# Performance work log

Hardware: AMD Instinct MI355X
Metric: run time of the kernel (lower is better)

## Reference

```python
import jax, jax.numpy as jnp
import numpy as np

N_NODES = 100000
N_EDGES = 1600000
C = 64


def _spline_conv(x, src, dst, u, w, root, bias, n_nodes):
    """SplineConv, dim=1, kernel_size=2, degree=1, open spline, aggr='mean'.

    For K=2, degree=1, pseudo u in [0,1]: basis = (1-u) on knot 0, u on knot 1.
    message_e = (1-u_e) * x[src_e] @ w[0] + u_e * x[src_e] @ w[1]
    Compute the two GEMMs at node level (N < E) then gather, which is
    mathematically identical and cheaper.
    """
    h0 = x @ w[0]  # [N, C]
    h1 = x @ w[1]  # [N, C]
    uc = u[:, None]  # [E, 1]
    msg = (1.0 - uc) * h0[src] + uc * h1[src]  # [E, C]
    agg = jax.ops.segment_sum(msg, dst, num_segments=n_nodes)  # [N, C]
    deg = jax.ops.segment_sum(jnp.ones_like(u), dst, num_segments=n_nodes)
    agg = agg / jnp.maximum(deg, 1.0)[:, None]  # mean aggregation
    return agg + x @ root + bias


def setup_inputs() -> dict:
    key = jax.random.key(0)
    ks = jax.random.split(key, 10)
    x = jax.random.normal(ks[0], (N_NODES, C), dtype=jnp.float32)
    edge_index = jax.random.randint(ks[1], (2, N_EDGES), 0, N_NODES, dtype=jnp.int64)
    edge_attr = jax.random.uniform(ks[2], (N_EDGES, 1), dtype=jnp.float32)
    s = 1.0 / np.sqrt(C)
    w1 = jax.random.uniform(ks[3], (2, C, C), jnp.float32, -s, s)
    root1 = jax.random.uniform(ks[4], (C, C), jnp.float32, -s, s)
    b1 = jnp.zeros((C,), jnp.float32)
    w2 = jax.random.uniform(ks[5], (2, C, C), jnp.float32, -s, s)
    root2 = jax.random.uniform(ks[6], (C, C), jnp.float32, -s, s)
    b2 = jnp.zeros((C,), jnp.float32)
    return {"x": x, "edge_index": edge_index, "edge_attr": edge_attr,
            "w1": w1, "root1": root1, "b1": b1,
            "w2": w2, "root2": root2, "b2": b2}


def reference(x, edge_index, edge_attr, w1, root1, b1, w2, root2, b2):
    src, dst = edge_index[0], edge_index[1]
    u = edge_attr[:, 0]
    n = x.shape[0]
    h = _spline_conv(x, src, dst, u, w1, root1, b1, n)
    h = _spline_conv(h, src, dst, u, w2, root2, b2, n)
    return h
```

## Files before the change

### kernel.cpp

```cpp
#include <hip/hip_runtime.h>

#define CDIM 64

typedef __attribute__((ext_vector_type(8))) short bf16x8;
typedef __attribute__((ext_vector_type(4))) float f32x4;

__device__ __forceinline__ short bf16r(float f) {
    unsigned a = __float_as_uint(f);
    a = (a + 0x7fffu + ((a >> 16) & 1u)) >> 16;
    return (short)a;
}
__device__ __forceinline__ unsigned bfpack(float lo, float hi) {
    unsigned a = __float_as_uint(lo);
    a = (a + 0x7fffu + ((a >> 16) & 1u)) >> 16;
    unsigned b = __float_as_uint(hi);
    b = (b + 0x7fffu + ((b >> 16) & 1u)) & 0xffff0000u;
    return a | b;
}

__global__ __launch_bounds__(256) void k_pack(const float* __restrict__ x,
                                              unsigned* __restrict__ xb32, size_t n2) {
    size_t t = (size_t)blockIdx.x * 256 + threadIdx.x;
    size_t stride = (size_t)gridDim.x * 256;
    for (size_t i = t; i < n2; i += stride) {
        float2 v = ((const float2*)x)[i];
        xb32[i] = bfpack(v.x, v.y);
    }
}

#define NPB_SHIFT 9
#define BKN (1 << NPB_SHIFT)
#define BPAD 10240
#define PART_CH 2048
#define RCAP 1536

__global__ __launch_bounds__(256) void k_prep(int* __restrict__ bkt_cursor, int n_buckets,
                                              const float* __restrict__ w1,
                                              const float* __restrict__ root1,
                                              const float* __restrict__ w2,
                                              const float* __restrict__ root2,
                                              short* __restrict__ wtg) {
    int tid = threadIdx.x;
    if (blockIdx.x == 0) {
        if (tid < n_buckets) bkt_cursor[tid] = tid * BPAD;
        return;
    }
    int l = blockIdx.x - 1;
    const float* s0 = l ? w2 : w1;
    const float* srcs[3] = {s0, s0 + 4096, l ? root2 : root1};
    short* o = wtg + (size_t)l * 3 * 4096;
    for (int i = tid; i < 12288; i += 256) {
        int m = i >> 12, r = i & 4095, k = r >> 6, n = r & 63;
        o[(m << 12) + (n << 6) + k] = bf16r(srcs[m][r]);
    }
}

__global__ __launch_bounds__(256) void k_part(const int* __restrict__ src,
                                              const int* __restrict__ dst,
                                              const float* __restrict__ u,
                                              int* __restrict__ bkt_cursor,
                                              unsigned long long* __restrict__ rec,
                                              int n_edges, int n_buckets) {
    __shared__ int cnt_s[256];
    __shared__ int off_s[256];
    int tid = threadIdx.x;
    cnt_s[tid] = 0;
    __syncthreads();
    int e0 = blockIdx.x * PART_CH + tid * 8;
    int d[8], s[8];
    float uu[8];
    if (e0 + 8 <= n_edges) {
        int4 d0 = *(const int4*)(dst + e0), d1 = *(const int4*)(dst + e0 + 4);
        int4 s0 = *(const int4*)(src + e0), s1 = *(const int4*)(src + e0 + 4);
        float4 u0 = *(const float4*)(u + e0), u1 = *(const float4*)(u + e0 + 4);
        d[0]=d0.x; d[1]=d0.y; d[2]=d0.z; d[3]=d0.w; d[4]=d1.x; d[5]=d1.y; d[6]=d1.z; d[7]=d1.w;
        s[0]=s0.x; s[1]=s0.y; s[2]=s0.z; s[3]=s0.w; s[4]=s1.x; s[5]=s1.y; s[6]=s1.z; s[7]=s1.w;
        uu[0]=u0.x; uu[1]=u0.y; uu[2]=u0.z; uu[3]=u0.w; uu[4]=u1.x; uu[5]=u1.y; uu[6]=u1.z; uu[7]=u1.w;
    } else {
#pragma unroll
        for (int i = 0; i < 8; ++i) {
            int e = e0 + i;
            bool ok = e < n_edges;
            d[i] = ok ? dst[e] : -1;
            s[i] = ok ? src[e] : 0;
            uu[i] = ok ? u[e] : 0.f;
        }
    }
#pragma unroll
    for (int i = 0; i < 8; ++i)
        if (d[i] >= 0) atomicAdd(&cnt_s[d[i] >> NPB_SHIFT], 1);
    __syncthreads();
    if (tid < n_buckets) {
        int c = cnt_s[tid];
        off_s[tid] = c ? atomicAdd(&bkt_cursor[tid], c) : 0;
    }
    __syncthreads();
#pragma unroll
    for (int i = 0; i < 8; ++i) {
        if (d[i] >= 0) {
            int b = d[i] >> NPB_SHIFT;
            int p = atomicAdd(&off_s[b], 1);
            unsigned uq = (unsigned)(uu[i] * 32767.0f + 0.5f);
            rec[p] = ((unsigned long long)(unsigned)d[i] << 32)
                   | (unsigned long long)(((unsigned)s[i] << 15) | uq);
        }
    }
}

__global__ __launch_bounds__(512) void k_fused(
        const unsigned* __restrict__ xb_in,
        const unsigned long long* __restrict__ rec,
        const int* __restrict__ bkt_cursor,
        const short* __restrict__ wb,
        const float* __restrict__ bias,
        float* __restrict__ out,
        unsigned short* __restrict__ xb_out,
        int n_nodes, int n_buckets) {
    __shared__ unsigned em_s[RCAP];
    __shared__ unsigned tmp_em[RCAP];
    __shared__ unsigned short tmp_d[RCAP];
    __shared__ int cnt_s[64];
    __shared__ int row_s[64];
    __shared__ int cur_s[64];
    __shared__ int nm_s;
    __shared__ __align__(16) unsigned gl[64][68];
    int tid = threadIdx.x;
    int blk = blockIdx.x;
    int b = (blk & 7) + 8 * (blk >> 6);
    int sub = (blk >> 3) & 7;
    if (b >= n_buckets) return;
    int lo = (b << NPB_SHIFT) + (sub << 6);
    int nrec = bkt_cursor[b] - b * BPAD;
    const unsigned long long* r0 = rec + (size_t)b * BPAD;
    const float inv15 = 1.0f / 32767.0f;

    if (tid < 64) cnt_s[tid] = 0;
    if (tid == 0) nm_s = 0;
    __syncthreads();
    for (int i = tid; i < nrec; i += 512) {
        unsigned long long r = r0[i];
        int rel = (int)(r >> 32) - lo;
        if ((unsigned)rel < 64u) {
            int p = atomicAdd(&nm_s, 1);
            if (p < RCAP) {
                tmp_em[p] = (unsigned)r;
                tmp_d[p] = (unsigned short)rel;
                atomicAdd(&cnt_s[rel], 1);
            }
        }
    }
    __syncthreads();
    if (tid < 64) row_s[tid] = cnt_s[tid];
    __syncthreads();
    for (int off = 1; off < 64; off <<= 1) {
        int t = (tid < 64 && tid >= off) ? row_s[tid - off] : 0;
        __syncthreads();
        if (tid < 64) row_s[tid] += t;
        __syncthreads();
    }
    if (tid < 64) {
        row_s[tid] -= cnt_s[tid];
        cur_s[tid] = row_s[tid];
    }
    __syncthreads();
    int nm = min(nm_s, RCAP);
    for (int i = tid; i < nm; i += 512) {
        int rel = tmp_d[i];
        int p = atomicAdd(&cur_s[rel], 1);
        em_s[p] = tmp_em[i];
    }
    __syncthreads();

    int qid = tid >> 4;
    int ql = tid & 15;
    for (int t = 0; t < 2; ++t) {
        int rel = qid * 2 + t;
        int start = row_s[rel];
        int cnt = cnt_s[rel];
        int end = start + cnt;
        float a0 = 0.f, a1 = 0.f, a2 = 0.f, a3 = 0.f;
        float b0 = 0.f, b1 = 0.f, b2 = 0.f, b3 = 0.f;
        int j = start;
        for (; j + 4 <= end; j += 4) {
            unsigned e[4]; uint2 v[4];
#pragma unroll
            for (int i = 0; i < 4; ++i) e[i] = em_s[j + i];
#pragma unroll
            for (int i = 0; i < 4; ++i)
                v[i] = *(const uint2*)(xb_in + (size_t)(e[i] >> 15) * 32 + 2 * ql);
#pragma unroll
            for (int i = 0; i < 4; ++i) {
                float uu = (float)(e[i] & 0x7fffu) * inv15;
                float wa = 1.0f - uu;
                float c0 = __uint_as_float(v[i].x << 16);
                float c1 = __uint_as_float(v[i].x & 0xffff0000u);
                float c2 = __uint_as_float(v[i].y << 16);
                float c3 = __uint_as_float(v[i].y & 0xffff0000u);
                a0 += wa * c0; a1 += wa * c1; a2 += wa * c2; a3 += wa * c3;
                b0 += uu * c0; b1 += uu * c1; b2 += uu * c2; b3 += uu * c3;
            }
        }
        if (j < end) {
            unsigned e[4]; uint2 v[4]; float m[4];
#pragma unroll
            for (int i = 0; i < 4; ++i) {
                int idx = j + i;
                bool ok = idx < end;
                e[i] = em_s[ok ? idx : (end - 1)];
                m[i] = ok ? 1.0f : 0.0f;
            }
#pragma unroll
            for (int i = 0; i < 4; ++i)
                v[i] = *(const uint2*)(xb_in + (size_t)(e[i] >> 15) * 32 + 2 * ql);
#pragma unroll
            for (int i = 0; i < 4; ++i) {
                float uu = (float)(e[i] & 0x7fffu) * inv15;
                float wa = (1.0f - uu) * m[i], wu = uu * m[i];
                float c0 = __uint_as_float(v[i].x << 16);
                float c1 = __uint_as_float(v[i].x & 0xffff0000u);
                float c2 = __uint_as_float(v[i].y << 16);
                float c3 = __uint_as_float(v[i].y & 0xffff0000u);
                a0 += wa * c0; a1 += wa * c1; a2 += wa * c2; a3 += wa * c3;
                b0 += wu * c0; b1 += wu * c1; b2 += wu * c2; b3 += wu * c3;
            }
        }
        float s = 1.0f / fmaxf((float)cnt, 1.0f);
        *(uint2*)&gl[rel][2 * ql] = make_uint2(bfpack(a0 * s, a1 * s), bfpack(a2 * s, a3 * s));
        *(uint2*)&gl[rel][32 + 2 * ql] = make_uint2(bfpack(b0 * s, b1 * s), bfpack(b2 * s, b3 * s));
    }
    __syncthreads();

    int wv = tid >> 6;
    int lane = tid & 63;
    int tile = wv & 3;
    int nthalf = wv >> 2;
    int quad = lane >> 4;
    int m16 = lane & 15;
    int rown = tile * 16 + m16;
    int arow = lo + rown;
    bool rowok = arow < n_nodes;
    const short* gp = (const short*)&gl[rown][0];
    const unsigned* xp = xb_in + (size_t)arow * 32;
    bf16x8 zf = {0, 0, 0, 0, 0, 0, 0, 0};
    bf16x8 aG0[2], aG1[2], aX[2];
#pragma unroll
    for (int kf = 0; kf < 2; ++kf) {
        aG0[kf] = *(const bf16x8*)(gp + kf * 32 + quad * 8);
        aG1[kf] = *(const bf16x8*)(gp + 64 + kf * 32 + quad * 8);
        aX[kf] = rowok ? *(const bf16x8*)(xp + kf * 16 + quad * 4) : zf;
    }
#pragma unroll
    for (int nh = 0; nh < 2; ++nh) {
        int nt = nthalf * 2 + nh;
        f32x4 accv = {0.f, 0.f, 0.f, 0.f};
#pragma unroll
        for (int kf = 0; kf < 2; ++kf) {
            int col = nt * 16 + m16;
            bf16x8 bw0 = *(const bf16x8*)(wb + (col << 6) + kf * 32 + quad * 8);
            bf16x8 bw1 = *(const bf16x8*)(wb + ((64 + col) << 6) + kf * 32 + quad * 8);
            bf16x8 bwR = *(const bf16x8*)(wb + ((128 + col) << 6) + kf * 32 + quad * 8);
            accv = __builtin_amdgcn_mfma_f32_16x16x32_bf16(aG0[kf], bw0, accv, 0, 0, 0);
            accv = __builtin_amdgcn_mfma_f32_16x16x32_bf16(aG1[kf], bw1, accv, 0, 0, 0);
            accv = __builtin_amdgcn_mfma_f32_16x16x32_bf16(aX[kf], bwR, accv, 0, 0, 0);
        }
        float bcol = bias[nt * 16 + m16];
#pragma unroll
        for (int r = 0; r < 4; ++r) {
            int node = lo + tile * 16 + quad * 4 + r;
            if (node < n_nodes) {
                size_t off = (size_t)node * CDIM + nt * 16 + m16;
                float o = accv[r] + bcol;
                if (out) out[off] = o;
                if (xb_out) xb_out[off] = (unsigned short)bf16r(o);
            }
        }
    }
}

extern "C" void kernel_launch(void* const* d_in, const int* in_sizes, int n_in,
                              void* d_out, int out_size, void* d_ws, size_t ws_size,
                              hipStream_t stream) {
    const float* x = (const float*)d_in[0];
    const int* edge_index = (const int*)d_in[1];
    const float* edge_attr = (const float*)d_in[2];
    const float* w1 = (const float*)d_in[3];
    const float* root1 = (const float*)d_in[4];
    const float* b1 = (const float*)d_in[5];
    const float* w2 = (const float*)d_in[6];
    const float* root2 = (const float*)d_in[7];
    const float* b2 = (const float*)d_in[8];

    int n_nodes = in_sizes[0] / CDIM;
    int n_edges = in_sizes[2];
    const int* src = edge_index;
    const int* dst = edge_index + n_edges;

    size_t F = (size_t)n_nodes * CDIM;
    int n_buckets = (n_nodes + BKN - 1) >> NPB_SHIFT;
    unsigned* xbA = (unsigned*)d_ws;
    unsigned* xbB = xbA + F / 2;
    int* bkt_cursor = (int*)(xbB + F / 2);
    uintptr_t p = (uintptr_t)(bkt_cursor + n_buckets);
    p = (p + 15) & ~(uintptr_t)15;
    short* wtg = (short*)p;
    p += (size_t)2 * 3 * 4096 * sizeof(short);
    p = (p + 15) & ~(uintptr_t)15;
    unsigned long long* rec = (unsigned long long*)p;
    float* out = (float*)d_out;

    int gP = (n_edges + PART_CH - 1) / PART_CH;
    int gF = 64 * ((n_buckets + 7) / 8);

    k_pack<<<2048, 256, 0, stream>>>(x, xbA, F / 2);
    k_prep<<<3, 256, 0, stream>>>(bkt_cursor, n_buckets, w1, root1, w2, root2, wtg);
    k_part<<<gP, 256, 0, stream>>>(src, dst, edge_attr, bkt_cursor, rec, n_edges, n_buckets);

    k_fused<<<gF, 512, 0, stream>>>(xbA, rec, bkt_cursor, wtg, b1,
                                    nullptr, (unsigned short*)xbB, n_nodes, n_buckets);
    k_fused<<<gF, 512, 0, stream>>>(xbB, rec, bkt_cursor, wtg + 3 * 4096, b2,
                                    out, nullptr, n_nodes, n_buckets);
}
```

Before: 271.5 us.

## Cache per-block sorted edge lists across layers and stage partition writes in LDS

The first fused layer now writes its sorted per-64-node edge list and row offsets/counts to global scratch. The second layer reads these back instead of rescanning the whole bucket's records, which avoids the repeated filter, scan and scatter work. Separately, the partition kernel computes a block-local prefix scan and stages records in shared memory, so global writes become contiguous runs per bucket instead of scattered single stores. The cost is extra global scratch, extra LDS in k_part, and second-layer edge-index reads that now come from global memory rather than LDS.

```diff
diff --git a/kernel.cpp b/kernel.cpp
--- a/kernel.cpp
+++ b/kernel.cpp
@@ -62,7 +62,12 @@
                                               unsigned long long* __restrict__ rec,
                                               int n_edges, int n_buckets) {
     __shared__ int cnt_s[256];
-    __shared__ int off_s[256];
+    __shared__ int excl_s[256];
+    __shared__ int cur_s[256];
+    __shared__ int goff_s[256];
+    __shared__ int tot_s;
+    __shared__ unsigned long long rec_s[PART_CH];
+    __shared__ int tgt_s[PART_CH];
     int tid = threadIdx.x;
     cnt_s[tid] = 0;
     __syncthreads();
@@ -90,21 +95,37 @@
     for (int i = 0; i < 8; ++i)
         if (d[i] >= 0) atomicAdd(&cnt_s[d[i] >> NPB_SHIFT], 1);
     __syncthreads();
-    if (tid < n_buckets) {
-        int c = cnt_s[tid];
-        off_s[tid] = c ? atomicAdd(&bkt_cursor[tid], c) : 0;
-    }
+    int c = cnt_s[tid];
+    excl_s[tid] = c;
+    __syncthreads();
+    for (int off = 1; off < 256; off <<= 1) {
+        int t = (tid >= off) ? excl_s[tid - off] : 0;
+        __syncthreads();
+        excl_s[tid] += t;
+        __syncthreads();
+    }
+    int excl = excl_s[tid] - c;
+    if (tid == 255) tot_s = excl_s[255];
+    __syncthreads();
+    excl_s[tid] = excl;
+    cur_s[tid] = excl;
+    goff_s[tid] = (tid < n_buckets && c) ? atomicAdd(&bkt_cursor[tid], c) : 0;
     __syncthreads();
 #pragma unroll
     for (int i = 0; i < 8; ++i) {
         if (d[i] >= 0) {
             int b = d[i] >> NPB_SHIFT;
-            int p = atomicAdd(&off_s[b], 1);
+            int p = atomicAdd(&cur_s[b], 1);
             unsigned uq = (unsigned)(uu[i] * 32767.0f + 0.5f);
-            rec[p] = ((unsigned long long)(unsigned)d[i] << 32)
-                   | (unsigned long long)(((unsigned)s[i] << 15) | uq);
-        }
-    }
+            rec_s[p] = ((unsigned long long)(unsigned)d[i] << 32)
+                     | (unsigned long long)(((unsigned)s[i] << 15) | uq);
+            tgt_s[p] = goff_s[b] + (p - excl_s[b]);
+        }
+    }
+    __syncthreads();
+    int tot = tot_s;
+    for (int i = tid; i < tot; i += 256)
+        rec[tgt_s[i]] = rec_s[i];
 }
 
 __global__ __launch_bounds__(512) void k_fused(
@@ -115,7 +136,9 @@
         const float* __restrict__ bias,
         float* __restrict__ out,
         unsigned short* __restrict__ xb_out,
-        int n_nodes, int n_buckets) {
+        unsigned* __restrict__ em_g,
+        unsigned* __restrict__ rowcnt_g,
+        int n_nodes, int n_buckets, int build) {
     __shared__ unsigned em_s[RCAP];
     __shared__ unsigned tmp_em[RCAP];
     __shared__ unsigned short tmp_d[RCAP];
@@ -130,47 +153,62 @@
     int sub = (blk >> 3) & 7;
     if (b >= n_buckets) return;
     int lo = (b << NPB_SHIFT) + (sub << 6);
-    int nrec = bkt_cursor[b] - b * BPAD;
-    const unsigned long long* r0 = rec + (size_t)b * BPAD;
+    int region = ((b << 3) + sub) * RCAP;
     const float inv15 = 1.0f / 32767.0f;
 
-    if (tid < 64) cnt_s[tid] = 0;
-    if (tid == 0) nm_s = 0;
-    __syncthreads();
-    for (int i = tid; i < nrec; i += 512) {
-        unsigned long long r = r0[i];
-        int rel = (int)(r >> 32) - lo;
-        if ((unsigned)rel < 64u) {
-            int p = atomicAdd(&nm_s, 1);
-            if (p < RCAP) {
-                tmp_em[p] = (unsigned)r;
-                tmp_d[p] = (unsigned short)rel;
-                atomicAdd(&cnt_s[rel], 1);
-            }
-        }
-    }
-    __syncthreads();
-    if (tid < 64) row_s[tid] = cnt_s[tid];
-    __syncthreads();
-    for (int off = 1; off < 64; off <<= 1) {
-        int t = (tid < 64 && tid >= off) ? row_s[tid - off] : 0;
-        __syncthreads();
-        if (tid < 64) row_s[tid] += t;
-        __syncthreads();
-    }
-    if (tid < 64) {
-        row_s[tid] -= cnt_s[tid];
-        cur_s[tid] = row_s[tid];
-    }
-    __syncthreads();
-    int nm = min(nm_s, RCAP);
-    for (int i = tid; i < nm; i += 512) {
-        int rel = tmp_d[i];
-        int p = atomicAdd(&cur_s[rel], 1);
-        em_s[p] = tmp_em[i];
-    }
-    __syncthreads();
-
+    if (build) {
+        int nrec = bkt_cursor[b] - b * BPAD;
+        const unsigned long long* r0 = rec + (size_t)b * BPAD;
+        if (tid < 64) cnt_s[tid] = 0;
+        if (tid == 0) nm_s = 0;
+        __syncthreads();
+        for (int i = tid; i < nrec; i += 512) {
+            unsigned long long r = r0[i];
+            int rel = (int)(r >> 32) - lo;
+            if ((unsigned)rel < 64u) {
+                int p = atomicAdd(&nm_s, 1);
+                if (p < RCAP) {
+                    tmp_em[p] = (unsigned)r;
+                    tmp_d[p] = (unsigned short)rel;
+                    atomicAdd(&cnt_s[rel], 1);
+                }
+            }
+        }
+        __syncthreads();
+        if (tid < 64) row_s[tid] = cnt_s[tid];
+        __syncthreads();
+        for (int off = 1; off < 64; off <<= 1) {
+            int t = (tid < 64 && tid >= off) ? row_s[tid - off] : 0;
+            __syncthreads();
+            if (tid < 64) row_s[tid] += t;
+            __syncthreads();
+        }
+        if (tid < 64) {
+            row_s[tid] -= cnt_s[tid];
+            cur_s[tid] = row_s[tid];
+        }
+        __syncthreads();
+        int nm = min(nm_s, RCAP);
+        for (int i = tid; i < nm; i += 512) {
+            int rel = tmp_d[i];
+            int p = atomicAdd(&cur_s[rel], 1);
+            em_s[p] = tmp_em[i];
+        }
+        __syncthreads();
+        if (tid < 64)
+            rowcnt_g[((b << 3) + sub) * 64 + tid] =
+                (unsigned)row_s[tid] | ((unsigned)cnt_s[tid] << 16);
+        for (int i = tid; i < nm; i += 512) em_g[region + i] = em_s[i];
+    } else {
+        if (tid < 64) {
+            unsigned rc = rowcnt_g[((b << 3) + sub) * 64 + tid];
+            row_s[tid] = (int)(rc & 0xffffu);
+            cnt_s[tid] = (int)(rc >> 16);
+        }
+        __syncthreads();
+    }
+
+    const unsigned* em = build ? (const unsigned*)&em_s[0] : (em_g + region);
     int qid = tid >> 4;
     int ql = tid & 15;
     for (int t = 0; t < 2; ++t) {
@@ -184,7 +222,7 @@
         for (; j + 4 <= end; j += 4) {
             unsigned e[4]; uint2 v[4];
 #pragma unroll
-            for (int i = 0; i < 4; ++i) e[i] = em_s[j + i];
+            for (int i = 0; i < 4; ++i) e[i] = em[j + i];
 #pragma unroll
             for (int i = 0; i < 4; ++i)
                 v[i] = *(const uint2*)(xb_in + (size_t)(e[i] >> 15) * 32 + 2 * ql);
@@ -206,7 +244,7 @@
             for (int i = 0; i < 4; ++i) {
                 int idx = j + i;
                 bool ok = idx < end;
-                e[i] = em_s[ok ? idx : (end - 1)];
+                e[i] = em[ok ? idx : (end - 1)];
                 m[i] = ok ? 1.0f : 0.0f;
             }
 #pragma unroll
@@ -297,6 +335,7 @@
 
     size_t F = (size_t)n_nodes * CDIM;
     int n_buckets = (n_nodes + BKN - 1) >> NPB_SHIFT;
+    int nb8 = n_buckets * 8;
     unsigned* xbA = (unsigned*)d_ws;
     unsigned* xbB = xbA + F / 2;
     int* bkt_cursor = (int*)(xbB + F / 2);
@@ -305,6 +344,11 @@
     short* wtg = (short*)p;
     p += (size_t)2 * 3 * 4096 * sizeof(short);
     p = (p + 15) & ~(uintptr_t)15;
+    unsigned* em_g = (unsigned*)p;
+    p += (size_t)nb8 * RCAP * sizeof(unsigned);
+    unsigned* rowcnt_g = (unsigned*)p;
+    p += (size_t)nb8 * 64 * sizeof(unsigned);
+    p = (p + 15) & ~(uintptr_t)15;
     unsigned long long* rec = (unsigned long long*)p;
     float* out = (float*)d_out;
 
@@ -316,7 +360,9 @@
     k_part<<<gP, 256, 0, stream>>>(src, dst, edge_attr, bkt_cursor, rec, n_edges, n_buckets);
 
     k_fused<<<gF, 512, 0, stream>>>(xbA, rec, bkt_cursor, wtg, b1,
-                                    nullptr, (unsigned short*)xbB, n_nodes, n_buckets);
+                                    nullptr, (unsigned short*)xbB,
+                                    em_g, rowcnt_g, n_nodes, n_buckets, 1);
     k_fused<<<gF, 512, 0, stream>>>(xbB, rec, bkt_cursor, wtg + 3 * 4096, b2,
-                                    out, nullptr, n_nodes, n_buckets);
-}
+                                    out, nullptr,
+                                    em_g, rowcnt_g, n_nodes, n_buckets, 0);
+}
```

Measured after the change: 263.0 us. 1.03x faster.
